# Performance work log

Hardware: AMD Instinct MI355X
Metric: run time of the kernel (lower is better)

## Reference

```python
import jax, jax.numpy as jnp
import numpy as np
import math

B, T, D, H, DM = 2, 2048, 1024, 16, 256
DK = D // H

def setup_inputs() -> dict:
    key = jax.random.key(0)
    ks = jax.random.split(key, 13)
    s = 0.02
    return {
        "Hx": jax.random.normal(ks[0], (B, D, T, 1), jnp.float32),
        "Hf": jax.random.normal(ks[1], (B, T, D), jnp.float32),
        "Gm": jax.random.normal(ks[2], (B, T, DM), jnp.float32),
        "Wg": jax.random.normal(ks[3], (T, DM), jnp.float32) * s,
        "bg": jax.random.normal(ks[4], (T,), jnp.float32) * s,
        "Wq": jax.random.normal(ks[5], (D, 2 * D), jnp.float32) * s,
        "bq": jax.random.normal(ks[6], (D,), jnp.float32) * s,
        "Wk": jax.random.normal(ks[7], (D, 2 * D), jnp.float32) * s,
        "bk": jax.random.normal(ks[8], (D,), jnp.float32) * s,
        "Wv": jax.random.normal(ks[9], (D, D), jnp.float32) * s,
        "bv": jax.random.normal(ks[10], (D,), jnp.float32) * s,
        "Wo": jax.random.normal(ks[11], (D, D), jnp.float32) * s,
        "bo": jax.random.normal(ks[12], (D,), jnp.float32) * s,
    }

def reference(Hx, Hf, Gm, Wg, bg, Wq, bq, Wk, bk, Wv, bv, Wo, bo):
    # Hx: (B, D, T, 1) -> (B, T, D)
    hx = jnp.transpose(Hx[..., 0], (0, 2, 1))
    h_cat = jnp.concatenate([hx, Hf], axis=-1)          # (B, T, 2D)
    Q = h_cat @ Wq.T + bq                               # (B, T, D)
    K = h_cat @ Wk.T + bk
    V = hx @ Wv.T + bv
    # split heads: (B, H, T, DK)
    Q = Q.reshape(B, T, H, DK).transpose(0, 2, 1, 3)
    K = K.reshape(B, T, H, DK).transpose(0, 2, 1, 3)
    V = V.reshape(B, T, H, DK).transpose(0, 2, 1, 3)
    scores = jnp.einsum('bhqd,bhkd->bhqk', Q, K) / math.sqrt(DK)
    bias = Gm @ Wg.T + bg                                # (B, T, T)
    scores = scores + bias[:, None, :, :]
    attn = jax.nn.softmax(scores, axis=-1)
    out = jnp.einsum('bhqk,bhkd->bhqd', attn, V)
    out = out.transpose(0, 2, 1, 3).reshape(B, T, D)
    return out @ Wo.T + bo
```

## Files before the change

### kernel.cpp

```cpp
#include <hip/hip_runtime.h>
#include <hip/hip_bf16.h>

using bf16 = __hip_bfloat16;
typedef __attribute__((ext_vector_type(8))) __bf16 bf16x8;
typedef __attribute__((ext_vector_type(4))) float f32x4;

#define GLB_AS(p) ((const __attribute__((address_space(1))) unsigned int*)(p))
#define LDS_AS(p) ((__attribute__((address_space(3))) unsigned int*)(p))

__device__ __forceinline__ void async_copy16(const void* g, void* l) {
  __builtin_amdgcn_global_load_lds(GLB_AS(g), LDS_AS(l), 16, 0, 0);
}

__device__ __forceinline__ f32x4 mfma16x16x32(bf16x8 a, bf16x8 b, f32x4 c) {
  return __builtin_amdgcn_mfma_f32_16x16x32_bf16(a, b, c, 0, 0, 0);
}

__device__ __forceinline__ float bfu2f(unsigned short u) {
  union { unsigned int i; float f; } x;
  x.i = (unsigned int)u << 16;
  return x.f;
}

#define LOG2E 1.44269504f

__global__ __launch_bounds__(256) void pack_hx(const float* __restrict__ Hx,
                                               bf16* __restrict__ hcat) {
  __shared__ float tile[64][65];
  const int t0 = blockIdx.x * 64, d0 = blockIdx.y * 64, b = blockIdx.z;
  const int c = threadIdx.x & 63, r0 = threadIdx.x >> 6;
#pragma unroll
  for (int i = 0; i < 16; ++i) {
    const int rd = r0 + i * 4;
    tile[rd][c] = Hx[((size_t)(b * 1024 + d0 + rd)) * 2048 + t0 + c];
  }
  __syncthreads();
#pragma unroll
  for (int i = 0; i < 16; ++i) {
    const int ct = r0 + i * 4;
    hcat[((size_t)(b * 2048 + t0 + ct)) * 2048 + d0 + c] =
        __float2bfloat16(tile[c][ct]);
  }
}

__global__ __launch_bounds__(256) void pack_all(
    const float* __restrict__ Hf, const float* __restrict__ Wq,
    const float* __restrict__ Wk, const float* __restrict__ Wv,
    const float* __restrict__ Wo, const float* __restrict__ Wg,
    const float* __restrict__ Gm, const float* __restrict__ bq,
    const float* __restrict__ bk, const float* __restrict__ bv,
    bf16* __restrict__ hcat, bf16* __restrict__ Wqkvb, bf16* __restrict__ Wob,
    bf16* __restrict__ Wgb, bf16* __restrict__ Gmb,
    float* __restrict__ qkvbias) {
  const int gid = blockIdx.x * 256 + threadIdx.x;
  const float* src = nullptr;
  bf16* dst = nullptr;
  int lg = 0, ldo = 0, off = 0, idx = 0;
  bool zero = false;
  if (gid < 1048576) { idx = gid; src = Hf; dst = hcat; lg = 8; ldo = 2048; off = 1024; }
  else if (gid < 1572864) { idx = gid - 1048576; src = Wq; dst = Wqkvb; lg = 9; ldo = 2048; }
  else if (gid < 2097152) { idx = gid - 1572864; src = Wk; dst = Wqkvb + (size_t)1024 * 2048; lg = 9; ldo = 2048; }
  else if (gid < 2359296) { idx = gid - 2097152; src = Wv; dst = Wqkvb + (size_t)2048 * 2048; lg = 8; ldo = 2048; }
  else if (gid < 2621440) { idx = gid - 2359296; zero = true; dst = Wqkvb + (size_t)2048 * 2048 + 1024; lg = 8; ldo = 2048; }
  else if (gid < 2883584) { idx = gid - 2621440; src = Wo; dst = Wob; lg = 8; ldo = 1024; }
  else if (gid < 3014656) { idx = gid - 2883584; src = Wg; dst = Wgb; lg = 6; ldo = 256; }
  else if (gid < 3276800) { idx = gid - 3014656; src = Gm; dst = Gmb; lg = 6; ldo = 256; }
  else if (gid < 3277056) { const int i = gid - 3276800; ((float4*)qkvbias)[i] = ((const float4*)bq)[i]; return; }
  else if (gid < 3277312) { const int i = gid - 3277056; ((float4*)(qkvbias + 1024))[i] = ((const float4*)bk)[i]; return; }
  else { const int i = gid - 3277312; ((float4*)(qkvbias + 2048))[i] = ((const float4*)bv)[i]; return; }
  const int row = idx >> lg, c = idx & ((1 << lg) - 1);
  bf16* o = dst + (size_t)row * ldo + off + c * 4;
  __align__(8) bf16 tmp[4];
  if (zero) {
    tmp[0] = tmp[1] = tmp[2] = tmp[3] = __float2bfloat16(0.f);
  } else {
    const float4 v = ((const float4*)src)[(size_t)idx];
    tmp[0] = __float2bfloat16(v.x); tmp[1] = __float2bfloat16(v.y);
    tmp[2] = __float2bfloat16(v.z); tmp[3] = __float2bfloat16(v.w);
  }
  *(ushort4*)o = *(const ushort4*)tmp;
}

__global__ __launch_bounds__(256) void gemm_qkv_bias(
    const bf16* __restrict__ hcat, const bf16* __restrict__ Wqkv,
    const float* __restrict__ qkvbias, const bf16* __restrict__ Gmb,
    const bf16* __restrict__ Wgb, const float* __restrict__ bg,
    bf16* __restrict__ QKb, bf16* __restrict__ Vt, bf16* __restrict__ biasS) {
  __shared__ __align__(16) bf16 As[2][128 * 64];
  __shared__ __align__(16) bf16 Bs[2][128 * 64];
  const int lin = blockIdx.x;
  const int xcd = lin & 7;
  const int kk = lin >> 3;
  const bool isqkv = kk < 96;
  int m_idx, n0;
  if (isqkv) {
    m_idx = kk / 3;
    n0 = (xcd * 3 + (kk - m_idx * 3)) * 128;
  } else {
    const int k2 = kk - 96;
    m_idx = k2 >> 1;
    n0 = (xcd * 2 + (k2 & 1)) * 128;
  }
  const int m0 = m_idx * 128;
  const bf16* A = isqkv ? hcat : Gmb;
  const bf16* W = isqkv ? Wqkv : Wgb;
  const float* biasv = isqkv ? qkvbias : bg;
  const int Kd = isqkv ? 2048 : 256;
  const int tid = threadIdx.x, lane = tid & 63, w = tid >> 6;
  const int wm = (w >> 1) * 64, wn = (w & 1) * 64;
  const int fr = lane & 15;
  const int ck = lane >> 4;

  f32x4 acc[4][4];
  const f32x4 fzero = {0.f, 0.f, 0.f, 0.f};
#pragma unroll
  for (int i = 0; i < 4; ++i)
#pragma unroll
    for (int j = 0; j < 4; ++j) acc[i][j] = fzero;

  auto stage = [&](int it, int buf) {
    const int k0 = it * 64;
#pragma unroll
    for (int is = 0; is < 4; ++is) {
      const int off = is * 4096 + w * 1024;
      const int row = (off >> 7) + (lane >> 3);
      const int sch = ((lane & 7) ^ (row & 7)) * 8;
      async_copy16(A + (size_t)(m0 + row) * Kd + k0 + sch,
                   (char*)As[buf] + off);
      async_copy16(W + (size_t)(n0 + row) * Kd + k0 + sch,
                   (char*)Bs[buf] + off);
    }
  };

  const int nit = Kd >> 6;
  stage(0, 0);
  __syncthreads();
  for (int it = 0; it < nit; ++it) {
    const int cur = it & 1;
    if (it + 1 < nit) stage(it + 1, cur ^ 1);
#pragma unroll
    for (int ks = 0; ks < 2; ++ks) {
      bf16x8 af[4], bfr[4];
#pragma unroll
      for (int i = 0; i < 4; ++i) {
        const int swk = (((ks * 4 + ck) ^ (fr & 7))) * 8;
        af[i] = *(const bf16x8*)(As[cur] + (wm + i * 16 + fr) * 64 + swk);
        bfr[i] = *(const bf16x8*)(Bs[cur] + (wn + i * 16 + fr) * 64 + swk);
      }
#pragma unroll
      for (int i = 0; i < 4; ++i)
#pragma unroll
        for (int j = 0; j < 4; ++j)
          acc[i][j] = mfma16x16x32(af[i], bfr[j], acc[i][j]);
    }
    __syncthreads();
  }
  const int erow = (lane >> 4) * 4;
  const int ecol = lane & 15;

  if (!isqkv) {
#pragma unroll
    for (int i = 0; i < 4; ++i) {
      const int gm0 = m0 + wm + i * 16 + erow;
#pragma unroll
      for (int j = 0; j < 4; ++j) {
        const int gn = n0 + wn + j * 16 + ecol;
        const float bv = biasv[gn];
#pragma unroll
        for (int r = 0; r < 4; ++r)
          biasS[(size_t)(gm0 + r) * 2048 + gn] =
              __float2bfloat16((acc[i][j][r] + bv) * LOG2E);
      }
    }
  } else if (n0 < 2048) {
    const float sc = (n0 < 1024) ? 0.125f * LOG2E : 1.0f;
#pragma unroll
    for (int i = 0; i < 4; ++i) {
      const int gm0 = m0 + wm + i * 16 + erow;
#pragma unroll
      for (int j = 0; j < 4; ++j) {
        const int gn = n0 + wn + j * 16 + ecol;
        const float bv = biasv[gn];
#pragma unroll
        for (int r = 0; r < 4; ++r)
          QKb[(size_t)(gm0 + r) * 2048 + gn] =
              __float2bfloat16((acc[i][j][r] + bv) * sc);
      }
    }
  } else {
#pragma unroll
    for (int i = 0; i < 4; ++i) {
      const int gm0 = m0 + wm + i * 16 + erow;
      const int bb = gm0 >> 11;
      const int t = gm0 & 2047;
#pragma unroll
      for (int j = 0; j < 4; ++j) {
        const int gn = n0 + wn + j * 16 + ecol;
        const float bv = biasv[gn];
        const int d = gn - 2048;
        __align__(8) bf16 tmp[4];
#pragma unroll
        for (int r = 0; r < 4; ++r)
          tmp[r] = __float2bfloat16(acc[i][j][r] + bv);
        *(ushort4*)(Vt + ((size_t)(bb * 1024 + d)) * 2048 + t) =
            *(const ushort4*)tmp;
      }
    }
  }
}

__global__ __launch_bounds__(256) void gemm_out(const bf16* __restrict__ A,
                                                const bf16* __restrict__ W,
                                                const float* __restrict__ biasv,
                                                float* __restrict__ C) {
  __shared__ __align__(16) bf16 As[2][128 * 64];
  __shared__ __align__(16) bf16 Bs[2][64 * 64];
  const int lin = blockIdx.x;
  const int xcd = lin & 7;
  const int kk = lin >> 3;
  const int m0 = (kk >> 1) * 128;
  const int n0 = (xcd * 2 + (kk & 1)) * 64;
  const int tid = threadIdx.x, lane = tid & 63, w = tid >> 6;
  const int wm = (w >> 1) * 64, wn = (w & 1) * 32;
  const int fr = lane & 15;
  const int ck = lane >> 4;

  f32x4 acc[4][2];
  const f32x4 fzero = {0.f, 0.f, 0.f, 0.f};
#pragma unroll
  for (int i = 0; i < 4; ++i)
#pragma unroll
    for (int j = 0; j < 2; ++j) acc[i][j] = fzero;

  auto stage = [&](int it, int buf) {
    const int k0 = it * 64;
#pragma unroll
    for (int is = 0; is < 4; ++is) {
      const int off = is * 4096 + w * 1024;
      const int row = (off >> 7) + (lane >> 3);
      const int sch = ((lane & 7) ^ (row & 7)) * 8;
      async_copy16(A + (size_t)(m0 + row) * 1024 + k0 + sch,
                   (char*)As[buf] + off);
      if (is < 2)
        async_copy16(W + (size_t)(n0 + row) * 1024 + k0 + sch,
                     (char*)Bs[buf] + off);
    }
  };

  stage(0, 0);
  __syncthreads();
  for (int it = 0; it < 16; ++it) {
    const int cur = it & 1;
    if (it + 1 < 16) stage(it + 1, cur ^ 1);
#pragma unroll
    for (int ks = 0; ks < 2; ++ks) {
      bf16x8 af[4], bfr[2];
      const int swk0 = (((ks * 4 + ck) ^ (fr & 7))) * 8;
#pragma unroll
      for (int i = 0; i < 4; ++i)
        af[i] = *(const bf16x8*)(As[cur] + (wm + i * 16 + fr) * 64 + swk0);
#pragma unroll
      for (int j = 0; j < 2; ++j)
        bfr[j] = *(const bf16x8*)(Bs[cur] + (wn + j * 16 + fr) * 64 + swk0);
#pragma unroll
      for (int i = 0; i < 4; ++i)
#pragma unroll
        for (int j = 0; j < 2; ++j)
          acc[i][j] = mfma16x16x32(af[i], bfr[j], acc[i][j]);
    }
    __syncthreads();
  }
  const int erow = (lane >> 4) * 4;
  const int ecol = lane & 15;
#pragma unroll
  for (int i = 0; i < 4; ++i) {
    const int gm0 = m0 + wm + i * 16 + erow;
#pragma unroll
    for (int j = 0; j < 2; ++j) {
      const int gn = n0 + wn + j * 16 + ecol;
      const float bv = biasv[gn];
#pragma unroll
      for (int r = 0; r < 4; ++r)
        C[(size_t)(gm0 + r) * 1024 + gn] = acc[i][j][r] + bv;
    }
  }
}

__global__ __launch_bounds__(256) void flash_attn(
    const bf16* __restrict__ Qm, const bf16* __restrict__ Km,
    const bf16* __restrict__ Vtm, const bf16* __restrict__ biasS,
    float* __restrict__ Op0, float* __restrict__ Op1,
    float* __restrict__ lpart) {
  __shared__ __align__(16) bf16 Ks[2][64 * 64];
  __shared__ __align__(16) bf16 Vs[2][64 * 64];
  __shared__ __align__(16) bf16 Ps[4 * 32 * 72];
  const int lin = blockIdx.x;
  const int xcd = lin & 7;
  const int kk = lin >> 3;
  const int cl = kk & 1;
  const int r2 = kk >> 1;
  const int half = r2 & 1;
  const int q0 = (r2 >> 1) * 128;
  const int combo = xcd * 2 + cl;
  const int hp = combo & 7;
  const int b = combo >> 3;
  const int tid = threadIdx.x, lane = tid & 63, w = tid >> 6;
  const int ql = lane & 15, qk = lane >> 4;
  const int T = 2048, D = 1024;
  const int sw0 = (qk ^ (ql & 7)) * 8;
  const int sw1 = ((qk + 4) ^ (ql & 7)) * 8;

  bf16x8 qf[2][2][2];
#pragma unroll
  for (int hh = 0; hh < 2; ++hh)
#pragma unroll
    for (int qt = 0; qt < 2; ++qt)
#pragma unroll
      for (int ks = 0; ks < 2; ++ks)
        qf[hh][qt][ks] = *(const bf16x8*)(
            Qm + (size_t)(b * T + q0 + w * 32 + qt * 16 + ql) * 2048 +
            (hp * 2 + hh) * 64 + ks * 32 + qk * 8);

  f32x4 acc[2][4][2];
  const f32x4 fzero = {0.f, 0.f, 0.f, 0.f};
#pragma unroll
  for (int hh = 0; hh < 2; ++hh)
#pragma unroll
    for (int dt = 0; dt < 4; ++dt)
#pragma unroll
      for (int qt = 0; qt < 2; ++qt) acc[hh][dt][qt] = fzero;
  float lp[2][2] = {{0.f, 0.f}, {0.f, 0.f}};

  const bf16* kbase0 = Km + (size_t)(b * T) * 2048 + (hp * 2) * 64;
  const bf16* vbase0 = Vtm + (size_t)(b * D + hp * 2 * 64) * 2048;
  const bf16* bb0 = biasS + (size_t)(b * T + q0 + w * 32 + ql) * 2048 + qk * 4;
  bf16* pb = Ps + w * 2304;

  for (int j = 0; j < 16; ++j) {
    const int jj = half * 16 + j;
    __syncthreads();
#pragma unroll
    for (int hh = 0; hh < 2; ++hh)
#pragma unroll
      for (int is = 0; is < 2; ++is) {
        const int off = is * 4096 + w * 1024;
        const int row = (off >> 7) + (lane >> 3);
        const int sch = ((lane & 7) ^ (row & 7)) * 8;
        async_copy16(kbase0 + (size_t)(jj * 64 + row) * 2048 + hh * 64 + sch,
                     (char*)Ks[hh] + off);
        async_copy16(vbase0 + (size_t)(hh * 64 + row) * 2048 + jj * 64 + sch,
                     (char*)Vs[hh] + off);
      }
    ushort4 bq[2][4];
#pragma unroll
    for (int qt = 0; qt < 2; ++qt)
#pragma unroll
      for (int jt = 0; jt < 4; ++jt)
        bq[qt][jt] = *(const ushort4*)(bb0 + (size_t)qt * 16 * 2048 + jj * 64 +
                                       jt * 16);
    __syncthreads();
#pragma unroll
    for (int hh = 0; hh < 2; ++hh) {
      const bf16* ksp = Ks[hh];
      const bf16* vsp = Vs[hh];
#pragma unroll
      for (int jt = 0; jt < 4; ++jt) {
        const bf16x8 kf0 = *(const bf16x8*)(ksp + (jt * 16 + ql) * 64 + sw0);
        const bf16x8 kf1 = *(const bf16x8*)(ksp + (jt * 16 + ql) * 64 + sw1);
#pragma unroll
        for (int qt = 0; qt < 2; ++qt) {
          f32x4 c;
          c[0] = bfu2f(bq[qt][jt].x); c[1] = bfu2f(bq[qt][jt].y);
          c[2] = bfu2f(bq[qt][jt].z); c[3] = bfu2f(bq[qt][jt].w);
          c = mfma16x16x32(kf0, qf[hh][qt][0], c);
          c = mfma16x16x32(kf1, qf[hh][qt][1], c);
          __align__(8) bf16 t4[4];
#pragma unroll
          for (int r = 0; r < 4; ++r) {
            const float pv = __builtin_amdgcn_exp2f(c[r]);
            lp[hh][qt] += pv;
            t4[r] = __float2bfloat16(pv);
          }
          *(ushort4*)(pb + (qt * 16 + ql) * 72 + jt * 16 + qk * 4) =
              *(const ushort4*)t4;
        }
      }
#pragma unroll
      for (int ks = 0; ks < 2; ++ks) {
        const bf16x8 pf0 = *(const bf16x8*)(pb + ql * 72 + ks * 32 + qk * 8);
        const bf16x8 pf1 =
            *(const bf16x8*)(pb + (16 + ql) * 72 + ks * 32 + qk * 8);
        const int sw = ks ? sw1 : sw0;
#pragma unroll
        for (int dt = 0; dt < 4; ++dt) {
          const bf16x8 vf = *(const bf16x8*)(vsp + (dt * 16 + ql) * 64 + sw);
          acc[hh][dt][0] = mfma16x16x32(pf0, vf, acc[hh][dt][0]);
          acc[hh][dt][1] = mfma16x16x32(pf1, vf, acc[hh][dt][1]);
        }
      }
    }
  }
#pragma unroll
  for (int hh = 0; hh < 2; ++hh)
#pragma unroll
    for (int qt = 0; qt < 2; ++qt) {
      lp[hh][qt] += __shfl_xor(lp[hh][qt], 16);
      lp[hh][qt] += __shfl_xor(lp[hh][qt], 32);
    }
  if (qk == 0) {
#pragma unroll
    for (int hh = 0; hh < 2; ++hh)
#pragma unroll
      for (int qt = 0; qt < 2; ++qt)
        lpart[half * 65536 + (b * 16 + hp * 2 + hh) * 2048 + q0 + w * 32 +
              qt * 16 + ql] = lp[hh][qt];
  }
  float* Op = half ? Op1 : Op0;
#pragma unroll
  for (int hh = 0; hh < 2; ++hh)
#pragma unroll
    for (int qt = 0; qt < 2; ++qt)
#pragma unroll
      for (int r = 0; r < 4; ++r) {
        const size_t orow =
            (size_t)(b * T + q0 + w * 32 + qt * 16 + qk * 4 + r);
#pragma unroll
        for (int dt = 0; dt < 4; ++dt)
          Op[orow * 1024 + (hp * 2 + hh) * 64 + dt * 16 + ql] =
              acc[hh][dt][qt][r];
      }
}

__global__ __launch_bounds__(256) void combine(const float* __restrict__ O0,
                                               const float* __restrict__ O1,
                                               const float* __restrict__ lpart,
                                               bf16* __restrict__ AOut) {
  const int idx = blockIdx.x * 256 + threadIdx.x;
  const int row = idx >> 8;
  const int col = (idx & 255) * 4;
  const int b = row >> 11, q = row & 2047, h = col >> 6;
  const int li = (b * 16 + h) * 2048 + q;
  const float inv = __builtin_amdgcn_rcpf(lpart[li] + lpart[65536 + li]);
  const float4 a = *(const float4*)(O0 + (size_t)row * 1024 + col);
  const float4 c = *(const float4*)(O1 + (size_t)row * 1024 + col);
  __align__(8) bf16 t[4] = {
      __float2bfloat16((a.x + c.x) * inv), __float2bfloat16((a.y + c.y) * inv),
      __float2bfloat16((a.z + c.z) * inv), __float2bfloat16((a.w + c.w) * inv)};
  *(ushort4*)(AOut + (size_t)row * 1024 + col) = *(const ushort4*)t;
}

extern "C" void kernel_launch(void* const* d_in, const int* in_sizes, int n_in,
                              void* d_out, int out_size, void* d_ws,
                              size_t ws_size, hipStream_t stream) {
  (void)in_sizes; (void)n_in; (void)out_size; (void)ws_size;
  const float* Hx = (const float*)d_in[0];
  const float* Hf = (const float*)d_in[1];
  const float* Gm = (const float*)d_in[2];
  const float* Wg = (const float*)d_in[3];
  const float* bg = (const float*)d_in[4];
  const float* Wq = (const float*)d_in[5];
  const float* bq = (const float*)d_in[6];
  const float* Wk = (const float*)d_in[7];
  const float* bk = (const float*)d_in[8];
  const float* Wv = (const float*)d_in[9];
  const float* bv = (const float*)d_in[10];
  const float* Wo = (const float*)d_in[11];
  const float* bo = (const float*)d_in[12];
  float* out = (float*)d_out;

  char* p = (char*)d_ws;
  bf16* hcat = (bf16*)p;   p += (size_t)4096 * 2048 * 2;
  bf16* QKb = (bf16*)p;    p += (size_t)4096 * 2048 * 2;
  bf16* Vtb = (bf16*)p;    p += (size_t)4096 * 1024 * 2;
  bf16* biasS = (bf16*)p;  p += (size_t)4096 * 2048 * 2;
  bf16* AOut = (bf16*)p;   p += (size_t)4096 * 1024 * 2;
  bf16* Wqkvb = (bf16*)p;  p += (size_t)3072 * 2048 * 2;
  bf16* Wob = (bf16*)p;    p += (size_t)1024 * 1024 * 2;
  bf16* Wgb = (bf16*)p;    p += (size_t)2048 * 256 * 2;
  bf16* Gmb = (bf16*)p;    p += (size_t)4096 * 256 * 2;
  float* qkvbias = (float*)p; p += (size_t)3072 * 4;
  float* Op1 = (float*)p;  p += (size_t)4096 * 1024 * 4;
  float* lpart = (float*)p; p += (size_t)2 * 65536 * 4;
  float* Op0 = (float*)hcat;

  pack_hx<<<dim3(32, 16, 2), 256, 0, stream>>>(Hx, hcat);
  pack_all<<<dim3(12803), 256, 0, stream>>>(Hf, Wq, Wk, Wv, Wo, Wg, Gm, bq, bk,
                                            bv, hcat, Wqkvb, Wob, Wgb, Gmb,
                                            qkvbias);
  gemm_qkv_bias<<<dim3(1280), 256, 0, stream>>>(hcat, Wqkvb, qkvbias, Gmb,
                                                Wgb, bg, QKb, Vtb, biasS);
  flash_attn<<<dim3(512), 256, 0, stream>>>(QKb, QKb + 1024, Vtb, biasS,
                                            Op0, Op1, lpart);
  combine<<<dim3(4096), 256, 0, stream>>>(Op0, Op1, lpart, AOut);
  gemm_out<<<dim3(512), 256, 0, stream>>>(AOut, Wob, bo, out);
}
```

Before: 294.0 us.

## Rewrite QKV/bias GEMM as 256x256 tile, 8-wave ping-pong pipelined kernel

The fused QKV and gate-bias GEMM moves from 128x128 tiles with 4 waves to 256x256 tiles with 8 waves. The K loop is split into quadrant stages, with async global-to-LDS copies interleaved between MFMA blocks under explicit barriers, waitcnts and setprio. Larger tiles raise arithmetic intensity and cut redundant global loads. The grid drops from 1280 to 320 blocks, which risks lower occupancy and tail imbalance, and the manual synchronisation is fragile.

After: 278.2 us, median of 2. -5.4%, faster.

```diff
diff --git a/kernel.cpp b/kernel.cpp
--- a/kernel.cpp
+++ b/kernel.cpp
@@ -81,132 +81,206 @@
   *(ushort4*)o = *(const ushort4*)tmp;
 }
 
-__global__ __launch_bounds__(256) void gemm_qkv_bias(
+__global__ __launch_bounds__(512, 2) void gemm_qkv_bias(
     const bf16* __restrict__ hcat, const bf16* __restrict__ Wqkv,
     const float* __restrict__ qkvbias, const bf16* __restrict__ Gmb,
     const bf16* __restrict__ Wgb, const float* __restrict__ bg,
     bf16* __restrict__ QKb, bf16* __restrict__ Vt, bf16* __restrict__ biasS) {
-  __shared__ __align__(16) bf16 As[2][128 * 64];
-  __shared__ __align__(16) bf16 Bs[2][128 * 64];
+  __shared__ __align__(16) bf16 AS[2][256][64];
+  __shared__ __align__(16) bf16 BS[2][256][64];
   const int lin = blockIdx.x;
-  const int xcd = lin & 7;
-  const int kk = lin >> 3;
-  const bool isqkv = kk < 96;
-  int m_idx, n0;
+  const bool isqkv = lin < 192;
+  int m0, n0, Kd, KT, nit2;
+  const bf16 *Ag, *Bg;
+  const float* biasv;
   if (isqkv) {
-    m_idx = kk / 3;
-    n0 = (xcd * 3 + (kk - m_idx * 3)) * 128;
+    const int xcd = lin & 7, kk = lin >> 3;
+    const int mloc = kk / 6, nloc = kk - mloc * 6;
+    m0 = ((xcd >> 1) * 4 + mloc) * 256;
+    n0 = ((xcd & 1) * 6 + nloc) * 256;
+    Ag = hcat; Bg = Wqkv; biasv = qkvbias;
+    Kd = 2048; KT = 32; nit2 = 16;
   } else {
-    const int k2 = kk - 96;
-    m_idx = k2 >> 1;
-    n0 = (xcd * 2 + (k2 & 1)) * 128;
-  }
-  const int m0 = m_idx * 128;
-  const bf16* A = isqkv ? hcat : Gmb;
-  const bf16* W = isqkv ? Wqkv : Wgb;
-  const float* biasv = isqkv ? qkvbias : bg;
-  const int Kd = isqkv ? 2048 : 256;
+    const int l2 = lin - 192;
+    m0 = (l2 >> 3) * 256;
+    n0 = (l2 & 7) * 256;
+    Ag = Gmb; Bg = Wgb; biasv = bg;
+    Kd = 256; KT = 4; nit2 = 2;
+  }
   const int tid = threadIdx.x, lane = tid & 63, w = tid >> 6;
-  const int wm = (w >> 1) * 64, wn = (w & 1) * 64;
-  const int fr = lane & 15;
-  const int ck = lane >> 4;
-
-  f32x4 acc[4][4];
+  const int w8 = w * 8, ln3 = lane >> 3, ch = lane & 7;
+  const int fr = lane & 15, ck = lane >> 4;
+  const int wm64 = (w >> 2) * 64;
+  const int wn32 = (w & 3) * 32;
+
+  f32x4 acc[8][4];
   const f32x4 fzero = {0.f, 0.f, 0.f, 0.f};
 #pragma unroll
-  for (int i = 0; i < 4; ++i)
+  for (int i = 0; i < 8; ++i)
 #pragma unroll
     for (int j = 0; j < 4; ++j) acc[i][j] = fzero;
 
-  auto stage = [&](int it, int buf) {
-    const int k0 = it * 64;
-#pragma unroll
-    for (int is = 0; is < 4; ++is) {
-      const int off = is * 4096 + w * 1024;
-      const int row = (off >> 7) + (lane >> 3);
-      const int sch = ((lane & 7) ^ (row & 7)) * 8;
-      async_copy16(A + (size_t)(m0 + row) * Kd + k0 + sch,
-                   (char*)As[buf] + off);
-      async_copy16(W + (size_t)(n0 + row) * Kd + k0 + sch,
-                   (char*)Bs[buf] + off);
+  auto stageA = [&](int buf, int mh, int kt) {
+    const int k0 = kt * 64;
+#pragma unroll
+    for (int l = 0; l < 2; ++l) {
+      const int rit = mh * 128 + l * 64 + w8 + ln3;
+      async_copy16(Ag + (size_t)(m0 + rit) * Kd + k0 + ((ch ^ ln3) << 3),
+                   (char*)&AS[buf][0][0] + ((mh * 128 + l * 64 + w8) << 7));
     }
   };
-
-  const int nit = Kd >> 6;
-  stage(0, 0);
-  __syncthreads();
-  for (int it = 0; it < nit; ++it) {
-    const int cur = it & 1;
-    if (it + 1 < nit) stage(it + 1, cur ^ 1);
-#pragma unroll
-    for (int ks = 0; ks < 2; ++ks) {
-      bf16x8 af[4], bfr[4];
-#pragma unroll
-      for (int i = 0; i < 4; ++i) {
-        const int swk = (((ks * 4 + ck) ^ (fr & 7))) * 8;
-        af[i] = *(const bf16x8*)(As[cur] + (wm + i * 16 + fr) * 64 + swk);
-        bfr[i] = *(const bf16x8*)(Bs[cur] + (wn + i * 16 + fr) * 64 + swk);
-      }
-#pragma unroll
-      for (int i = 0; i < 4; ++i)
-#pragma unroll
-        for (int j = 0; j < 4; ++j)
-          acc[i][j] = mfma16x16x32(af[i], bfr[j], acc[i][j]);
-    }
-    __syncthreads();
-  }
-  const int erow = (lane >> 4) * 4;
-  const int ecol = lane & 15;
-
+  auto stageB = [&](int buf, int nh, int kt) {
+    const int k0 = kt * 64;
+#pragma unroll
+    for (int l = 0; l < 2; ++l) {
+      const int rit = nh * 128 + l * 64 + w8 + ln3;
+      async_copy16(Bg + (size_t)(n0 + rit) * Kd + k0 + ((ch ^ ln3) << 3),
+                   (char*)&BS[buf][0][0] + ((nh * 128 + l * 64 + w8) << 7));
+    }
+  };
+
+  bf16x8 af[4][2], bA[2][2], bB[2][2];
+  auto ldA = [&](int buf, int mh) {
+#pragma unroll
+    for (int i = 0; i < 4; ++i)
+#pragma unroll
+      for (int ks = 0; ks < 2; ++ks)
+        af[i][ks] = *(const bf16x8*)(
+            &AS[buf][mh * 128 + wm64 + i * 16 + fr][0] +
+            (((ks * 4 + ck) ^ (fr & 7)) << 3));
+  };
+  auto ldB = [&](bf16x8 (&dst)[2][2], int buf, int nh) {
+#pragma unroll
+    for (int j = 0; j < 2; ++j)
+#pragma unroll
+      for (int ks = 0; ks < 2; ++ks)
+        dst[j][ks] = *(const bf16x8*)(
+            &BS[buf][nh * 128 + wn32 + j * 16 + fr][0] +
+            (((ks * 4 + ck) ^ (fr & 7)) << 3));
+  };
+
+#define BAR() __builtin_amdgcn_s_barrier()
+#define LGKM0() asm volatile("s_waitcnt lgkmcnt(0)" ::: "memory")
+#define MMAQ(MH, NH, BF)                                                      \
+  __builtin_amdgcn_s_setprio(1);                                              \
+  _Pragma("unroll") for (int i_ = 0; i_ < 4; ++i_) {                          \
+    _Pragma("unroll") for (int j_ = 0; j_ < 2; ++j_) {                        \
+      acc[(MH) * 4 + i_][(NH) * 2 + j_] = mfma16x16x32(                       \
+          af[i_][0], BF[j_][0], acc[(MH) * 4 + i_][(NH) * 2 + j_]);           \
+      acc[(MH) * 4 + i_][(NH) * 2 + j_] = mfma16x16x32(                       \
+          af[i_][1], BF[j_][1], acc[(MH) * 4 + i_][(NH) * 2 + j_]);           \
+    }                                                                         \
+  }                                                                           \
+  __builtin_amdgcn_s_setprio(0);
+
+  stageA(0, 0, 0); stageB(0, 0, 0); stageB(0, 1, 0); stageA(0, 1, 0);
+  stageA(1, 0, 1); stageB(1, 0, 1);
+  asm volatile("s_waitcnt vmcnt(4)" ::: "memory");
+  BAR();
+
+  for (int it = 0; it < nit2; ++it) {
+    const int kodd = 2 * it + 1;
+    const int kn0 = (2 * it + 2 < KT) ? 2 * it + 2 : KT - 1;
+    const int kn1 = (2 * it + 3 < KT) ? 2 * it + 3 : KT - 1;
+
+    ldA(0, 0); ldB(bA, 0, 0);
+    stageB(1, 1, kodd);
+    asm volatile("s_waitcnt lgkmcnt(8)");
+    BAR(); LGKM0();
+    MMAQ(0, 0, bA);
+    BAR();
+    ldB(bB, 0, 1);
+    stageA(1, 1, kodd);
+    BAR(); LGKM0();
+    MMAQ(0, 1, bB);
+    BAR();
+    ldA(0, 1);
+    stageA(0, 0, kn0);
+    BAR(); LGKM0();
+    MMAQ(1, 0, bA);
+    BAR();
+    stageB(0, 0, kn0);
+    asm volatile("s_waitcnt vmcnt(4)" ::: "memory");
+    BAR();
+    MMAQ(1, 1, bB);
+    BAR();
+    ldA(1, 0); ldB(bA, 1, 0);
+    stageB(0, 1, kn0);
+    asm volatile("s_waitcnt lgkmcnt(8)");
+    BAR(); LGKM0();
+    MMAQ(0, 0, bA);
+    BAR();
+    ldB(bB, 1, 1);
+    stageA(0, 1, kn0);
+    BAR(); LGKM0();
+    MMAQ(0, 1, bB);
+    BAR();
+    ldA(1, 1);
+    stageA(1, 0, kn1);
+    BAR(); LGKM0();
+    MMAQ(1, 0, bA);
+    BAR();
+    stageB(1, 0, kn1);
+    asm volatile("s_waitcnt vmcnt(4)" ::: "memory");
+    BAR();
+    MMAQ(1, 1, bB);
+    BAR();
+  }
+  asm volatile("s_waitcnt vmcnt(0)" ::: "memory");
+
+  const int erow = (lane >> 4) * 4, ecol = lane & 15;
   if (!isqkv) {
 #pragma unroll
-    for (int i = 0; i < 4; ++i) {
-      const int gm0 = m0 + wm + i * 16 + erow;
-#pragma unroll
-      for (int j = 0; j < 4; ++j) {
-        const int gn = n0 + wn + j * 16 + ecol;
+    for (int ai = 0; ai < 8; ++ai) {
+      const int gm0 = m0 + (ai >> 2) * 128 + wm64 + (ai & 3) * 16 + erow;
+#pragma unroll
+      for (int bj = 0; bj < 4; ++bj) {
+        const int gn = n0 + (bj >> 1) * 128 + wn32 + (bj & 1) * 16 + ecol;
         const float bv = biasv[gn];
 #pragma unroll
         for (int r = 0; r < 4; ++r)
           biasS[(size_t)(gm0 + r) * 2048 + gn] =
-              __float2bfloat16((acc[i][j][r] + bv) * LOG2E);
+              __float2bfloat16((acc[ai][bj][r] + bv) * LOG2E);
       }
     }
   } else if (n0 < 2048) {
     const float sc = (n0 < 1024) ? 0.125f * LOG2E : 1.0f;
 #pragma unroll
-    for (int i = 0; i < 4; ++i) {
-      const int gm0 = m0 + wm + i * 16 + erow;
-#pragma unroll
-      for (int j = 0; j < 4; ++j) {
-        const int gn = n0 + wn + j * 16 + ecol;
+    for (int ai = 0; ai < 8; ++ai) {
+      const int gm0 = m0 + (ai >> 2) * 128 + wm64 + (ai & 3) * 16 + erow;
+#pragma unroll
+      for (int bj = 0; bj < 4; ++bj) {
+        const int gn = n0 + (bj >> 1) * 128 + wn32 + (bj & 1) * 16 + ecol;
         const float bv = biasv[gn];
 #pragma unroll
         for (int r = 0; r < 4; ++r)
           QKb[(size_t)(gm0 + r) * 2048 + gn] =
-              __float2bfloat16((acc[i][j][r] + bv) * sc);
+              __float2bfloat16((acc[ai][bj][r] + bv) * sc);
       }
     }
   } else {
 #pragma unroll
-    for (int i = 0; i < 4; ++i) {
-      const int gm0 = m0 + wm + i * 16 + erow;
+    for (int ai = 0; ai < 8; ++ai) {
+      const int gm0 = m0 + (ai >> 2) * 128 + wm64 + (ai & 3) * 16 + erow;
       const int bb = gm0 >> 11;
       const int t = gm0 & 2047;
 #pragma unroll
-      for (int j = 0; j < 4; ++j) {
-        const int gn = n0 + wn + j * 16 + ecol;
+      for (int bj = 0; bj < 4; ++bj) {
+        const int gn = n0 + (bj >> 1) * 128 + wn32 + (bj & 1) * 16 + ecol;
         const float bv = biasv[gn];
         const int d = gn - 2048;
         __align__(8) bf16 tmp[4];
 #pragma unroll
         for (int r = 0; r < 4; ++r)
-          tmp[r] = __float2bfloat16(acc[i][j][r] + bv);
+          tmp[r] = __float2bfloat16(acc[ai][bj][r] + bv);
         *(ushort4*)(Vt + ((size_t)(bb * 1024 + d)) * 2048 + t) =
             *(const ushort4*)tmp;
       }
     }
   }
+#undef MMAQ
+#undef LGKM0
+#undef BAR
 }
 
 __global__ __launch_bounds__(256) void gemm_out(const bf16* __restrict__ A,
@@ -487,8 +561,8 @@
   pack_all<<<dim3(12803), 256, 0, stream>>>(Hf, Wq, Wk, Wv, Wo, Wg, Gm, bq, bk,
                                             bv, hcat, Wqkvb, Wob, Wgb, Gmb,
                                             qkvbias);
-  gemm_qkv_bias<<<dim3(1280), 256, 0, stream>>>(hcat, Wqkvb, qkvbias, Gmb,
-                                                Wgb, bg, QKb, Vtb, biasS);
+  gemm_qkv_bias<<<dim3(320), 512, 0, stream>>>(hcat, Wqkvb, qkvbias, Gmb,
+                                               Wgb, bg, QKb, Vtb, biasS);
   flash_attn<<<dim3(512), 256, 0, stream>>>(QKb, QKb + 1024, Vtb, biasS,
                                             Op0, Op1, lpart);
   combine<<<dim3(4096), 256, 0, stream>>>(Op0, Op1, lpart, AOut);
```
